# Kernel tuning notes

Measured on AMD Instinct MI355X. Metric: run time of the kernel, lower is better.

The kernel has to match this reference:

```python
import jax, jax.numpy as jnp
import numpy as np

N = 4096
BATCH = 256
N_IO = 16
EPS = 1.1920929e-07  # torch RMSNorm default eps = finfo(float32).eps


def setup_inputs() -> dict:
    key = jax.random.key(0)
    k_x, k_w = jax.random.split(key)
    x_input = jax.random.normal(k_x, (BATCH, N), dtype=jnp.float32)
    # orthogonal init for W
    a = jax.random.normal(k_w, (N, N), dtype=jnp.float32)
    q, r = jnp.linalg.qr(a)
    W = q * jnp.sign(jnp.diag(r))[None, :]
    B = jnp.zeros((N,), dtype=jnp.float32)
    input_scale = jnp.ones((N_IO,), dtype=jnp.float32)
    output_scale = jnp.ones((N_IO,), dtype=jnp.float32)
    norm_weight = jnp.ones((N,), dtype=jnp.float32)  # RMSNorm elementwise affine
    input_pos = jnp.arange(N_IO, dtype=jnp.int32)            # ids 0..15
    output_pos = jnp.arange(N_IO, dtype=jnp.int32) + (N - N_IO)  # ids 4080..4095
    return {
        "x_input": x_input, "W": W, "B": B,
        "input_scale": input_scale, "output_scale": output_scale,
        "norm_weight": norm_weight,
        "input_pos": input_pos, "output_pos": output_pos,
        "steps": 16,
    }


def reference(x_input, W, B, input_scale, output_scale, norm_weight,
              input_pos, output_pos, steps):
    # dropout is identity in eval mode (rate 0.0)
    def step(h, inj):
        signal = h @ W + B + inj                      # [batch, N]
        a = jnp.tanh(signal)
        ms = jnp.mean(a * a, axis=-1, keepdims=True)
        return a * jax.lax.rsqrt(ms + EPS) * norm_weight

    # pulse mode: scaled input injected only at t == 0
    inj0 = x_input.at[:, input_pos].multiply(input_scale)
    h0 = jnp.zeros_like(x_input)                      # fresh state
    h1 = step(h0, inj0)

    def body(h, _):
        hn = step(h, 0.0)
        return hn, hn

    h_final, rest = jax.lax.scan(body, h1, None, length=steps - 1)  # rest: [steps-1, batch, N]
    outs = jnp.concatenate([h1[:, None, :], jnp.swapaxes(rest, 0, 1)], axis=1)  # [batch, steps, N]
    outs = outs.at[:, :, output_pos].multiply(output_scale)
    return outs, h_final
```

## Files before the change

kernel.cpp:

```cpp
#include <hip/hip_runtime.h>
#include <hip/hip_bf16.h>

#define BATCH 256
#define NDIM  4096
#define STEPS 16
#define EPS_RMS 1.1920929e-07f

typedef _Float16 f16x8 __attribute__((ext_vector_type(8)));
typedef float  f32x4  __attribute__((ext_vector_type(4)));
typedef unsigned short u16x4 __attribute__((ext_vector_type(4)));
typedef unsigned int   u32x4 __attribute__((ext_vector_type(4)));

#define AS1 __attribute__((address_space(1)))
#define AS3 __attribute__((address_space(3)))
#define GLDS16(gp, lp) __builtin_amdgcn_global_load_lds( \
    (const AS1 void*)(gp), (AS3 void*)(lp), 16, 0, 0)
#define SBAR() do { asm volatile("" ::: "memory"); \
                    __builtin_amdgcn_s_barrier();  \
                    asm volatile("" ::: "memory"); } while (0)

__device__ __forceinline__ unsigned short f2h(float f) {
  _Float16 h = (_Float16)f;
  union { _Float16 h; unsigned short u; } v; v.h = h; return v.u;
}

__device__ __forceinline__ float block_reduce_sum_512(float v) {
  __shared__ float ws[8];
  __shared__ float tot;
  #pragma unroll
  for (int off = 32; off > 0; off >>= 1) v += __shfl_down(v, off, 64);
  int lane = threadIdx.x & 63, w = threadIdx.x >> 6;
  if (lane == 0) ws[w] = v;
  __syncthreads();
  if (threadIdx.x == 0) {
    float t = 0.f;
    #pragma unroll
    for (int i = 0; i < 8; ++i) t += ws[i];
    tot = t;
  }
  __syncthreads();
  return tot;
}

__global__ __launch_bounds__(256) void transpose_w(
    const float* __restrict__ W, unsigned short* __restrict__ Wt) {
  __shared__ float tile[64][65];
  int n0 = blockIdx.x * 64;
  int k0 = blockIdx.y * 64;
  int t = threadIdx.x;
  int r = t >> 4, c4 = (t & 15) * 4;
  #pragma unroll
  for (int p = 0; p < 4; ++p) {
    f32x4 v = *(const f32x4*)(W + (size_t)(k0 + r + 16 * p) * NDIM + n0 + c4);
    tile[r + 16 * p][c4 + 0] = v[0];
    tile[r + 16 * p][c4 + 1] = v[1];
    tile[r + 16 * p][c4 + 2] = v[2];
    tile[r + 16 * p][c4 + 3] = v[3];
  }
  __syncthreads();
  #pragma unroll
  for (int p = 0; p < 4; ++p) {
    int nr = r + 16 * p;
    u16x4 o;
    #pragma unroll
    for (int j = 0; j < 4; ++j) o[j] = f2h(tile[c4 + j][nr]);
    *(u16x4*)(Wt + (size_t)(n0 + nr) * NDIM + k0 + c4) = o;
  }
}

__global__ void init_colmul(const float* __restrict__ iscale,
                            const float* __restrict__ oscale,
                            const int* __restrict__ ipos, const int* __restrict__ opos,
                            float* __restrict__ icm, float* __restrict__ ocm) {
  int c = blockIdx.x * 256 + threadIdx.x;
  if (c >= NDIM) return;
  float iv = 1.f, ov = 1.f;
  #pragma unroll
  for (int i = 0; i < 16; ++i) {
    if (ipos[i] == c) iv *= iscale[i];
    if (opos[i] == c) ov *= oscale[i];
  }
  icm[c] = iv; ocm[c] = ov;
}

__global__ __launch_bounds__(512) void step0_kernel(
    const float* __restrict__ x, const float* __restrict__ bias,
    const float* __restrict__ icm, const float* __restrict__ nw,
    const float* __restrict__ ocm,
    unsigned short* __restrict__ hbuf, float* __restrict__ out) {
  int row = blockIdx.x;
  int tid = threadIdx.x;
  const float* xr = x + (size_t)row * NDIM;
  float a[8];
  float sq = 0.f;
  #pragma unroll
  for (int p = 0; p < 2; ++p) {
    int c = p * 2048 + tid * 4;
    f32x4 xv = *(const f32x4*)(xr + c);
    f32x4 bv = *(const f32x4*)(bias + c);
    f32x4 ic = *(const f32x4*)(icm + c);
    #pragma unroll
    for (int j = 0; j < 4; ++j) {
      float av = tanhf(bv[j] + xv[j] * ic[j]);
      a[p * 4 + j] = av;
      sq += av * av;
    }
  }
  float tot = block_reduce_sum_512(sq);
  float scale = rsqrtf(tot * (1.0f / NDIM) + EPS_RMS);
  unsigned short* hrow = hbuf + (size_t)row * NDIM;
  float* orow = out + (size_t)row * STEPS * NDIM;
  #pragma unroll
  for (int p = 0; p < 2; ++p) {
    int c = p * 2048 + tid * 4;
    f32x4 nv = *(const f32x4*)(nw + c);
    f32x4 oc = *(const f32x4*)(ocm + c);
    u16x4 hs; f32x4 os;
    #pragma unroll
    for (int j = 0; j < 4; ++j) {
      float h = a[p * 4 + j] * scale * nv[j];
      hs[j] = f2h(h);
      os[j] = h * oc[j];
    }
    *(u16x4*)(hrow + c) = hs;
    *(f32x4*)(orow + c) = os;
  }
}

__global__ __launch_bounds__(256, 2) void gemm_kernel(
    const unsigned short* __restrict__ A,
    const unsigned short* __restrict__ Bt,
    float* __restrict__ pbuf) {
  __shared__ __align__(16) unsigned short As[2][64 * 64];
  __shared__ __align__(16) unsigned short Bs[2][128 * 64];
  const int tid = threadIdx.x;
  const int n0 = blockIdx.x * 128;
  const int m0 = blockIdx.y * 64;
  const int ks = blockIdx.z;
  const int kbase = ks * 1024;
  const int wave = tid >> 6, lane = tid & 63;
  const int wm = (wave >> 1) * 32, wn = (wave & 1) * 64;
  const int l15 = lane & 15;
  const int g = lane >> 4;
  const int q = l15 & 7;
  const int rho = lane >> 3;
  const int koff = ((lane & 7) ^ rho) * 8;

  const unsigned short* aP[2];
  const unsigned short* bP[4];
  #pragma unroll
  for (int i = 0; i < 2; ++i)
    aP[i] = A + (size_t)(m0 + wave * 16 + i * 8 + rho) * NDIM + kbase + koff;
  #pragma unroll
  for (int i = 0; i < 4; ++i)
    bP[i] = Bt + (size_t)(n0 + wave * 32 + i * 8 + rho) * NDIM + kbase + koff;

  f32x4 acc[2][4];
  f32x4 zero = {0.f, 0.f, 0.f, 0.f};
  #pragma unroll
  for (int i = 0; i < 2; ++i)
    #pragma unroll
    for (int j = 0; j < 4; ++j) acc[i][j] = zero;

  #pragma unroll
  for (int i = 0; i < 2; ++i)
    GLDS16(aP[i], &As[0][(wave * 16 + i * 8) * 64]);
  #pragma unroll
  for (int i = 0; i < 4; ++i)
    GLDS16(bP[i], &Bs[0][(wave * 32 + i * 8) * 64]);

  for (int it = 0; it < 16; ++it) {
    const int p = it & 1;
    SBAR();
    if (it < 15) {
      const int kb = (it + 1) * 64;
      #pragma unroll
      for (int i = 0; i < 2; ++i)
        GLDS16(aP[i] + kb, &As[1 - p][(wave * 16 + i * 8) * 64]);
      #pragma unroll
      for (int i = 0; i < 4; ++i)
        GLDS16(bP[i] + kb, &Bs[1 - p][(wave * 32 + i * 8) * 64]);
      asm volatile("s_waitcnt vmcnt(6)" ::: "memory");
    } else {
      asm volatile("s_waitcnt vmcnt(0)" ::: "memory");
    }
    SBAR();
    #pragma unroll
    for (int kk = 0; kk < 2; ++kk) {
      f16x8 af[2], bfr[4];
      #pragma unroll
      for (int mf = 0; mf < 2; ++mf) {
        int row = wm + mf * 16 + l15;
        af[mf] = *(const f16x8*)&As[p][row * 64 + (((kk << 2) + g) ^ q) * 8];
      }
      #pragma unroll
      for (int nf = 0; nf < 4; ++nf) {
        int row = wn + nf * 16 + l15;
        bfr[nf] = *(const f16x8*)&Bs[p][row * 64 + (((kk << 2) + g) ^ q) * 8];
      }
      #pragma unroll
      for (int mf = 0; mf < 2; ++mf)
        #pragma unroll
        for (int nf = 0; nf < 4; ++nf)
          acc[mf][nf] = __builtin_amdgcn_mfma_f32_16x16x32_f16(af[mf], bfr[nf], acc[mf][nf], 0, 0, 0);
    }
  }

  float* pout = pbuf + (size_t)ks * BATCH * NDIM;
  const int crow = (lane >> 4) * 4;
  #pragma unroll
  for (int mf = 0; mf < 2; ++mf) {
    #pragma unroll
    for (int nf = 0; nf < 4; ++nf) {
      int col = n0 + wn + nf * 16 + l15;
      #pragma unroll
      for (int r = 0; r < 4; ++r) {
        int row = m0 + wm + mf * 16 + crow + r;
        pout[(size_t)row * NDIM + col] = acc[mf][nf][r];
      }
    }
  }
}

__global__ __launch_bounds__(512) void normalize_kernel(
    const float* __restrict__ pbuf, const float* __restrict__ bias,
    const float* __restrict__ nw, const float* __restrict__ ocm,
    unsigned short* __restrict__ hbuf, float* __restrict__ out,
    float* __restrict__ hfin, int t, int is_last) {
  const size_t SL = (size_t)BATCH * NDIM;
  int row = blockIdx.x;
  int tid = threadIdx.x;
  const float* p0 = pbuf + (size_t)row * NDIM;
  float a[8];
  float sq = 0.f;
  #pragma unroll
  for (int p = 0; p < 2; ++p) {
    int c = p * 2048 + tid * 4;
    f32x4 s = *(const f32x4*)(p0 + c);
    s += *(const f32x4*)(p0 + SL + c);
    s += *(const f32x4*)(p0 + 2 * SL + c);
    s += *(const f32x4*)(p0 + 3 * SL + c);
    f32x4 bv = *(const f32x4*)(bias + c);
    #pragma unroll
    for (int j = 0; j < 4; ++j) {
      float av = tanhf(s[j] + bv[j]);
      a[p * 4 + j] = av;
      sq += av * av;
    }
  }
  float tot = block_reduce_sum_512(sq);
  float scale = rsqrtf(tot * (1.0f / NDIM) + EPS_RMS);
  unsigned short* hrow = hbuf + (size_t)row * NDIM;
  float* orow = out + ((size_t)row * STEPS + t) * NDIM;
  #pragma unroll
  for (int p = 0; p < 2; ++p) {
    int c = p * 2048 + tid * 4;
    f32x4 nv = *(const f32x4*)(nw + c);
    f32x4 oc = *(const f32x4*)(ocm + c);
    u16x4 hs; f32x4 os; f32x4 hv;
    #pragma unroll
    for (int j = 0; j < 4; ++j) {
      float h = a[p * 4 + j] * scale * nv[j];
      hv[j] = h;
      hs[j] = f2h(h);
      os[j] = h * oc[j];
    }
    *(u16x4*)(hrow + c) = hs;
    *(f32x4*)(orow + c) = os;
    if (is_last) *(f32x4*)(hfin + (size_t)row * NDIM + c) = hv;
  }
}

extern "C" void kernel_launch(void* const* d_in, const int* in_sizes, int n_in,
                              void* d_out, int out_size, void* d_ws, size_t ws_size,
                              hipStream_t stream) {
  (void)in_sizes; (void)n_in; (void)out_size; (void)ws_size;
  const float* x      = (const float*)d_in[0];
  const float* W      = (const float*)d_in[1];
  const float* Bb     = (const float*)d_in[2];
  const float* iscale = (const float*)d_in[3];
  const float* oscale = (const float*)d_in[4];
  const float* nw     = (const float*)d_in[5];
  const int* ipos = (const int*)d_in[6];
  const int* opos = (const int*)d_in[7];

  char* ws = (char*)d_ws;
  unsigned short* Wt   = (unsigned short*)(ws);
  unsigned short* hbuf = (unsigned short*)(ws + 33554432);
  float* icm           = (float*)(ws + 35651584);
  float* ocm           = (float*)(ws + 35667968);
  float* pbuf          = (float*)(ws + 35684352);

  float* out  = (float*)d_out;
  float* hfin = out + (size_t)BATCH * STEPS * NDIM;

  hipLaunchKernelGGL(transpose_w, dim3(64, 64), dim3(256), 0, stream, W, Wt);
  hipLaunchKernelGGL(init_colmul, dim3(16), dim3(256), 0, stream,
                     iscale, oscale, ipos, opos, icm, ocm);
  hipLaunchKernelGGL(step0_kernel, dim3(256), dim3(512), 0, stream,
                     x, Bb, icm, nw, ocm, hbuf, out);
  for (int t = 1; t < STEPS; ++t) {
    hipLaunchKernelGGL(gemm_kernel, dim3(32, 4, 4), dim3(256), 0, stream,
                       hbuf, Wt, pbuf);
    hipLaunchKernelGGL(normalize_kernel, dim3(256), dim3(512), 0, stream,
                       pbuf, Bb, nw, ocm, hbuf, out, hfin, t, (t == STEPS - 1) ? 1 : 0);
  }
}
```

Measured before the change: 362.4 us.

## Fuse GEMM with tanh/RMS epilogue using deferred row normalization and atomic row sums

Replaces the split-K GEMM plus separate normalize kernel with one fused kernel per step. Each step stores the un-normalized tanh activations in fp16, accumulates squared sums per row with atomics, and applies the previous step's RMS scale inside the epilogue. This is valid because the row scale factors out of the matmul. Outputs for step t-1 are written lazily from the stored activations, and a final kernel handles the last step. This removes the fp32 partial-sum buffer traffic and half the launches. In exchange it drops split-K, so each step runs only 256 blocks of 128 threads over the full K=4096 loop, which may underutilize the GPU, and it relies on atomics.

```diff
diff --git a/kernel.cpp b/kernel.cpp
--- a/kernel.cpp
+++ b/kernel.cpp
@@ -9,6 +9,7 @@
 typedef _Float16 f16x8 __attribute__((ext_vector_type(8)));
 typedef float  f32x4  __attribute__((ext_vector_type(4)));
 typedef unsigned short u16x4 __attribute__((ext_vector_type(4)));
+typedef unsigned short u16x8 __attribute__((ext_vector_type(8)));
 typedef unsigned int   u32x4 __attribute__((ext_vector_type(4)));
 
 #define AS1 __attribute__((address_space(1)))
@@ -23,6 +24,9 @@
   _Float16 h = (_Float16)f;
   union { _Float16 h; unsigned short u; } v; v.h = h; return v.u;
 }
+__device__ __forceinline__ float h2f(unsigned short u) {
+  union { unsigned short u; _Float16 h; } v; v.u = u; return (float)v.h;
+}
 
 __device__ __forceinline__ float block_reduce_sum_512(float v) {
   __shared__ float ws[8];
@@ -71,9 +75,11 @@
 __global__ void init_colmul(const float* __restrict__ iscale,
                             const float* __restrict__ oscale,
                             const int* __restrict__ ipos, const int* __restrict__ opos,
-                            float* __restrict__ icm, float* __restrict__ ocm) {
+                            float* __restrict__ icm, float* __restrict__ ocm,
+                            float* __restrict__ rowsum) {
   int c = blockIdx.x * 256 + threadIdx.x;
   if (c >= NDIM) return;
+  rowsum[c] = 0.f;
   float iv = 1.f, ov = 1.f;
   #pragma unroll
   for (int i = 0; i < 16; ++i) {
@@ -86,8 +92,7 @@
 __global__ __launch_bounds__(512) void step0_kernel(
     const float* __restrict__ x, const float* __restrict__ bias,
     const float* __restrict__ icm, const float* __restrict__ nw,
-    const float* __restrict__ ocm,
-    unsigned short* __restrict__ hbuf, float* __restrict__ out) {
+    unsigned short* __restrict__ A0, float* __restrict__ rs0) {
   int row = blockIdx.x;
   int tid = threadIdx.x;
   const float* xr = x + (size_t)row * NDIM;
@@ -107,167 +112,185 @@
     }
   }
   float tot = block_reduce_sum_512(sq);
-  float scale = rsqrtf(tot * (1.0f / NDIM) + EPS_RMS);
-  unsigned short* hrow = hbuf + (size_t)row * NDIM;
-  float* orow = out + (size_t)row * STEPS * NDIM;
+  if (tid == 0) rs0[row] = tot;
+  unsigned short* arow = A0 + (size_t)row * NDIM;
   #pragma unroll
   for (int p = 0; p < 2; ++p) {
     int c = p * 2048 + tid * 4;
     f32x4 nv = *(const f32x4*)(nw + c);
-    f32x4 oc = *(const f32x4*)(ocm + c);
-    u16x4 hs; f32x4 os;
-    #pragma unroll
-    for (int j = 0; j < 4; ++j) {
-      float h = a[p * 4 + j] * scale * nv[j];
-      hs[j] = f2h(h);
-      os[j] = h * oc[j];
-    }
-    *(u16x4*)(hrow + c) = hs;
-    *(f32x4*)(orow + c) = os;
-  }
-}
-
-__global__ __launch_bounds__(256, 2) void gemm_kernel(
-    const unsigned short* __restrict__ A,
-    const unsigned short* __restrict__ Bt,
-    float* __restrict__ pbuf) {
+    u16x4 hs;
+    #pragma unroll
+    for (int j = 0; j < 4; ++j) hs[j] = f2h(a[p * 4 + j] * nv[j]);
+    *(u16x4*)(arow + c) = hs;
+  }
+}
+
+__global__ __launch_bounds__(128) void fused_step(
+    const unsigned short* __restrict__ Aprev,
+    unsigned short* __restrict__ Acur,
+    const unsigned short* __restrict__ Wt,
+    const float* __restrict__ bias, const float* __restrict__ nw,
+    const float* __restrict__ ocm,
+    const float* __restrict__ rs_prev, float* __restrict__ rs_cur,
+    float* __restrict__ out, int tm1) {
   __shared__ __align__(16) unsigned short As[2][64 * 64];
-  __shared__ __align__(16) unsigned short Bs[2][128 * 64];
+  __shared__ __align__(16) unsigned short Bs[2][64 * 64];
+  __shared__ float scale_s[64];
+
   const int tid = threadIdx.x;
-  const int n0 = blockIdx.x * 128;
+  const int n0 = blockIdx.x * 64;
   const int m0 = blockIdx.y * 64;
-  const int ks = blockIdx.z;
-  const int kbase = ks * 1024;
   const int wave = tid >> 6, lane = tid & 63;
-  const int wm = (wave >> 1) * 32, wn = (wave & 1) * 64;
+  const int wn = wave * 32;
   const int l15 = lane & 15;
   const int g = lane >> 4;
   const int q = l15 & 7;
-  const int rho = lane >> 3;
-  const int koff = ((lane & 7) ^ rho) * 8;
-
-  const unsigned short* aP[2];
+  const int srow = tid >> 3;
+  const int sch = tid & 7;
+  const int koff = (sch ^ (srow & 7)) * 8;
+
+  const unsigned short* aP[4];
   const unsigned short* bP[4];
   #pragma unroll
-  for (int i = 0; i < 2; ++i)
-    aP[i] = A + (size_t)(m0 + wave * 16 + i * 8 + rho) * NDIM + kbase + koff;
-  #pragma unroll
-  for (int i = 0; i < 4; ++i)
-    bP[i] = Bt + (size_t)(n0 + wave * 32 + i * 8 + rho) * NDIM + kbase + koff;
-
-  f32x4 acc[2][4];
+  for (int i = 0; i < 4; ++i) {
+    aP[i] = Aprev + (size_t)(m0 + i * 16 + srow) * NDIM + koff;
+    bP[i] = Wt + (size_t)(n0 + i * 16 + srow) * NDIM + koff;
+  }
+
+  f32x4 acc[4][2];
   f32x4 zero = {0.f, 0.f, 0.f, 0.f};
   #pragma unroll
-  for (int i = 0; i < 2; ++i)
-    #pragma unroll
-    for (int j = 0; j < 4; ++j) acc[i][j] = zero;
-
-  #pragma unroll
-  for (int i = 0; i < 2; ++i)
-    GLDS16(aP[i], &As[0][(wave * 16 + i * 8) * 64]);
-  #pragma unroll
-  for (int i = 0; i < 4; ++i)
-    GLDS16(bP[i], &Bs[0][(wave * 32 + i * 8) * 64]);
-
-  for (int it = 0; it < 16; ++it) {
+  for (int i = 0; i < 4; ++i) { acc[i][0] = zero; acc[i][1] = zero; }
+
+  #pragma unroll
+  for (int i = 0; i < 4; ++i) {
+    GLDS16(aP[i], &As[0][(i * 16 + srow) * 64 + sch * 8]);
+    GLDS16(bP[i], &Bs[0][(i * 16 + srow) * 64 + sch * 8]);
+  }
+
+  for (int it = 0; it < 64; ++it) {
     const int p = it & 1;
     SBAR();
-    if (it < 15) {
-      const int kb = (it + 1) * 64;
-      #pragma unroll
-      for (int i = 0; i < 2; ++i)
-        GLDS16(aP[i] + kb, &As[1 - p][(wave * 16 + i * 8) * 64]);
-      #pragma unroll
-      for (int i = 0; i < 4; ++i)
-        GLDS16(bP[i] + kb, &Bs[1 - p][(wave * 32 + i * 8) * 64]);
-      asm volatile("s_waitcnt vmcnt(6)" ::: "memory");
-    } else {
-      asm volatile("s_waitcnt vmcnt(0)" ::: "memory");
-    }
+    {
+      const int kb = (it < 63 ? (it + 1) : 63) * 64;
+      #pragma unroll
+      for (int i = 0; i < 4; ++i) {
+        GLDS16(aP[i] + kb, &As[1 - p][(i * 16 + srow) * 64 + sch * 8]);
+        GLDS16(bP[i] + kb, &Bs[1 - p][(i * 16 + srow) * 64 + sch * 8]);
+      }
+    }
+    asm volatile("s_waitcnt vmcnt(8)" ::: "memory");
     SBAR();
     #pragma unroll
     for (int kk = 0; kk < 2; ++kk) {
-      f16x8 af[2], bfr[4];
-      #pragma unroll
-      for (int mf = 0; mf < 2; ++mf) {
-        int row = wm + mf * 16 + l15;
-        af[mf] = *(const f16x8*)&As[p][row * 64 + (((kk << 2) + g) ^ q) * 8];
+      f16x8 af[4], bfr[2];
+      #pragma unroll
+      for (int mf = 0; mf < 4; ++mf)
+        af[mf] = *(const f16x8*)&As[p][(mf * 16 + l15) * 64 + (((kk << 2) + g) ^ q) * 8];
+      #pragma unroll
+      for (int nf = 0; nf < 2; ++nf)
+        bfr[nf] = *(const f16x8*)&Bs[p][(wn + nf * 16 + l15) * 64 + (((kk << 2) + g) ^ q) * 8];
+      #pragma unroll
+      for (int mf = 0; mf < 4; ++mf)
+        #pragma unroll
+        for (int nf = 0; nf < 2; ++nf)
+          acc[mf][nf] = __builtin_amdgcn_mfma_f32_16x16x32_f16(af[mf], bfr[nf], acc[mf][nf], 0, 0, 0);
+    }
+  }
+
+  __syncthreads();
+  if (tid < 64) scale_s[tid] = rsqrtf(rs_prev[m0 + tid] * (1.0f / NDIM) + EPS_RMS);
+  __syncthreads();
+
+  float bv[2], nwv[2];
+  #pragma unroll
+  for (int nf = 0; nf < 2; ++nf) {
+    bv[nf] = bias[n0 + wn + nf * 16 + l15];
+    nwv[nf] = nw[n0 + wn + nf * 16 + l15];
+  }
+  unsigned short* Ast = &As[0][0];
+
+  #pragma unroll
+  for (int mf = 0; mf < 4; ++mf) {
+    #pragma unroll
+    for (int r = 0; r < 4; ++r) {
+      int rl = mf * 16 + g * 4 + r;
+      float rp = scale_s[rl];
+      float s2 = 0.f;
+      #pragma unroll
+      for (int nf = 0; nf < 2; ++nf) {
+        float a = tanhf(acc[mf][nf][r] * rp + bv[nf]);
+        s2 += a * a;
+        Ast[rl * 64 + wn + nf * 16 + l15] = f2h(a * nwv[nf]);
       }
-      #pragma unroll
-      for (int nf = 0; nf < 4; ++nf) {
-        int row = wn + nf * 16 + l15;
-        bfr[nf] = *(const f16x8*)&Bs[p][row * 64 + (((kk << 2) + g) ^ q) * 8];
+      s2 += __shfl_xor(s2, 1, 64);
+      s2 += __shfl_xor(s2, 2, 64);
+      s2 += __shfl_xor(s2, 4, 64);
+      s2 += __shfl_xor(s2, 8, 64);
+      if (l15 == 0) atomicAdd(rs_cur + m0 + rl, s2);
+    }
+  }
+  __syncthreads();
+
+  {
+    int cl = (tid & 7) * 8;
+    #pragma unroll
+    for (int rd = 0; rd < 4; ++rd) {
+      int rl = rd * 16 + (tid >> 3);
+      *(u16x8*)(Acur + (size_t)(m0 + rl) * NDIM + n0 + cl) = *(u16x8*)&Ast[rl * 64 + cl];
+    }
+  }
+
+  {
+    int cl = (tid & 7) * 8;
+    f32x4 oc0 = *(const f32x4*)(ocm + n0 + cl);
+    f32x4 oc1 = *(const f32x4*)(ocm + n0 + cl + 4);
+    #pragma unroll
+    for (int rd = 0; rd < 4; ++rd) {
+      int rl = rd * 16 + (tid >> 3);
+      u16x8 av = *(const u16x8*)(Aprev + (size_t)(m0 + rl) * NDIM + n0 + cl);
+      float rp = scale_s[rl];
+      f32x4 o0, o1;
+      #pragma unroll
+      for (int j = 0; j < 4; ++j) {
+        o0[j] = h2f(av[j]) * rp * oc0[j];
+        o1[j] = h2f(av[j + 4]) * rp * oc1[j];
       }
-      #pragma unroll
-      for (int mf = 0; mf < 2; ++mf)
-        #pragma unroll
-        for (int nf = 0; nf < 4; ++nf)
-          acc[mf][nf] = __builtin_amdgcn_mfma_f32_16x16x32_f16(af[mf], bfr[nf], acc[mf][nf], 0, 0, 0);
-    }
-  }
-
-  float* pout = pbuf + (size_t)ks * BATCH * NDIM;
-  const int crow = (lane >> 4) * 4;
-  #pragma unroll
-  for (int mf = 0; mf < 2; ++mf) {
-    #pragma unroll
-    for (int nf = 0; nf < 4; ++nf) {
-      int col = n0 + wn + nf * 16 + l15;
-      #pragma unroll
-      for (int r = 0; r < 4; ++r) {
-        int row = m0 + wm + mf * 16 + crow + r;
-        pout[(size_t)row * NDIM + col] = acc[mf][nf][r];
-      }
-    }
-  }
-}
-
-__global__ __launch_bounds__(512) void normalize_kernel(
-    const float* __restrict__ pbuf, const float* __restrict__ bias,
-    const float* __restrict__ nw, const float* __restrict__ ocm,
-    unsigned short* __restrict__ hbuf, float* __restrict__ out,
-    float* __restrict__ hfin, int t, int is_last) {
-  const size_t SL = (size_t)BATCH * NDIM;
+      float* orow = out + ((size_t)(m0 + rl) * STEPS + tm1) * NDIM + n0 + cl;
+      *(f32x4*)orow = o0;
+      *(f32x4*)(orow + 4) = o1;
+    }
+  }
+}
+
+__global__ __launch_bounds__(256) void final_kernel(
+    const unsigned short* __restrict__ Alast, const float* __restrict__ rs15,
+    const float* __restrict__ ocm,
+    float* __restrict__ out, float* __restrict__ hfin) {
   int row = blockIdx.x;
   int tid = threadIdx.x;
-  const float* p0 = pbuf + (size_t)row * NDIM;
-  float a[8];
-  float sq = 0.f;
-  #pragma unroll
-  for (int p = 0; p < 2; ++p) {
-    int c = p * 2048 + tid * 4;
-    f32x4 s = *(const f32x4*)(p0 + c);
-    s += *(const f32x4*)(p0 + SL + c);
-    s += *(const f32x4*)(p0 + 2 * SL + c);
-    s += *(const f32x4*)(p0 + 3 * SL + c);
-    f32x4 bv = *(const f32x4*)(bias + c);
-    #pragma unroll
-    for (int j = 0; j < 4; ++j) {
-      float av = tanhf(s[j] + bv[j]);
-      a[p * 4 + j] = av;
-      sq += av * av;
-    }
-  }
-  float tot = block_reduce_sum_512(sq);
-  float scale = rsqrtf(tot * (1.0f / NDIM) + EPS_RMS);
-  unsigned short* hrow = hbuf + (size_t)row * NDIM;
-  float* orow = out + ((size_t)row * STEPS + t) * NDIM;
-  #pragma unroll
-  for (int p = 0; p < 2; ++p) {
-    int c = p * 2048 + tid * 4;
-    f32x4 nv = *(const f32x4*)(nw + c);
-    f32x4 oc = *(const f32x4*)(ocm + c);
-    u16x4 hs; f32x4 os; f32x4 hv;
-    #pragma unroll
-    for (int j = 0; j < 4; ++j) {
-      float h = a[p * 4 + j] * scale * nv[j];
-      hv[j] = h;
-      hs[j] = f2h(h);
-      os[j] = h * oc[j];
-    }
-    *(u16x4*)(hrow + c) = hs;
-    *(f32x4*)(orow + c) = os;
-    if (is_last) *(f32x4*)(hfin + (size_t)row * NDIM + c) = hv;
+  float rp = rsqrtf(rs15[row] * (1.0f / NDIM) + EPS_RMS);
+  const unsigned short* ar = Alast + (size_t)row * NDIM;
+  float* orow = out + ((size_t)row * STEPS + (STEPS - 1)) * NDIM;
+  float* frow = hfin + (size_t)row * NDIM;
+  #pragma unroll
+  for (int j = 0; j < 2; ++j) {
+    int c = tid * 16 + j * 8;
+    u16x8 av = *(const u16x8*)(ar + c);
+    f32x4 oc0 = *(const f32x4*)(ocm + c);
+    f32x4 oc1 = *(const f32x4*)(ocm + c + 4);
+    f32x4 h0, h1, o0, o1;
+    #pragma unroll
+    for (int k = 0; k < 4; ++k) {
+      h0[k] = h2f(av[k]) * rp;
+      h1[k] = h2f(av[k + 4]) * rp;
+      o0[k] = h0[k] * oc0[k];
+      o1[k] = h1[k] * oc1[k];
+    }
+    *(f32x4*)(orow + c) = o0;
+    *(f32x4*)(orow + c + 4) = o1;
+    *(f32x4*)(frow + c) = h0;
+    *(f32x4*)(frow + c + 4) = h1;
   }
 }
 
@@ -285,24 +308,28 @@
   const int* opos = (const int*)d_in[7];
 
   char* ws = (char*)d_ws;
-  unsigned short* Wt   = (unsigned short*)(ws);
-  unsigned short* hbuf = (unsigned short*)(ws + 33554432);
-  float* icm           = (float*)(ws + 35651584);
-  float* ocm           = (float*)(ws + 35667968);
-  float* pbuf          = (float*)(ws + 35684352);
+  unsigned short* Wt    = (unsigned short*)(ws);
+  unsigned short* abuf0 = (unsigned short*)(ws + 33554432);
+  unsigned short* abuf1 = (unsigned short*)(ws + 35651584);
+  float* icm            = (float*)(ws + 37748736);
+  float* ocm            = (float*)(ws + 37765120);
+  float* rowsum         = (float*)(ws + 37781504);
 
   float* out  = (float*)d_out;
   float* hfin = out + (size_t)BATCH * STEPS * NDIM;
 
   hipLaunchKernelGGL(transpose_w, dim3(64, 64), dim3(256), 0, stream, W, Wt);
   hipLaunchKernelGGL(init_colmul, dim3(16), dim3(256), 0, stream,
-                     iscale, oscale, ipos, opos, icm, ocm);
+                     iscale, oscale, ipos, opos, icm, ocm, rowsum);
   hipLaunchKernelGGL(step0_kernel, dim3(256), dim3(512), 0, stream,
-                     x, Bb, icm, nw, ocm, hbuf, out);
+                     x, Bb, icm, nw, abuf0, rowsum);
   for (int t = 1; t < STEPS; ++t) {
-    hipLaunchKernelGGL(gemm_kernel, dim3(32, 4, 4), dim3(256), 0, stream,
-                       hbuf, Wt, pbuf);
-    hipLaunchKernelGGL(normalize_kernel, dim3(256), dim3(512), 0, stream,
-                       pbuf, Bb, nw, ocm, hbuf, out, hfin, t, (t == STEPS - 1) ? 1 : 0);
-  }
-}
+    const unsigned short* Ap = ((t - 1) & 1) ? abuf1 : abuf0;
+    unsigned short* Ac = (t & 1) ? abuf1 : abuf0;
+    hipLaunchKernelGGL(fused_step, dim3(64, 4), dim3(128), 0, stream,
+                       Ap, Ac, Wt, Bb, nw, ocm,
+                       rowsum + (t - 1) * 256, rowsum + t * 256, out, t - 1);
+  }
+  hipLaunchKernelGGL(final_kernel, dim3(256), dim3(256), 0, stream,
+                     abuf1, rowsum + 15 * 256, ocm, out, hfin);
+}
```

Result: slower. 959.2 us (+164.7%).

## Enlarge GEMM tile to 128x128 and use deeper split-K when workspace allows

Applied to the files above, without the earlier changes.

The GEMM block tile grows from 64x128 to 128x128, so each wave computes 64x64 with 16 accumulators. This doubles operand reuse per LDS load and halves how often W is refetched across M blocks. To keep enough blocks in flight, split-K rises to 8 when the workspace is large enough, and the normalize kernel sums a variable number of partial slices. The cost is more partial-sum traffic in fp32, higher register pressure, and a runtime loop in the reduction.

```diff
diff --git a/kernel.cpp b/kernel.cpp
--- a/kernel.cpp
+++ b/kernel.cpp
@@ -130,66 +130,68 @@
 __global__ __launch_bounds__(256, 2) void gemm_kernel(
     const unsigned short* __restrict__ A,
     const unsigned short* __restrict__ Bt,
-    float* __restrict__ pbuf) {
-  __shared__ __align__(16) unsigned short As[2][64 * 64];
+    float* __restrict__ pbuf,
+    int kslen) {
+  __shared__ __align__(16) unsigned short As[2][128 * 64];
   __shared__ __align__(16) unsigned short Bs[2][128 * 64];
   const int tid = threadIdx.x;
   const int n0 = blockIdx.x * 128;
-  const int m0 = blockIdx.y * 64;
+  const int m0 = blockIdx.y * 128;
   const int ks = blockIdx.z;
-  const int kbase = ks * 1024;
+  const int kbase = ks * kslen;
+  const int nit = kslen >> 6;
   const int wave = tid >> 6, lane = tid & 63;
-  const int wm = (wave >> 1) * 32, wn = (wave & 1) * 64;
+  const int wm = (wave >> 1) * 64, wn = (wave & 1) * 64;
   const int l15 = lane & 15;
   const int g = lane >> 4;
   const int q = l15 & 7;
-  const int rho = lane >> 3;
-  const int koff = ((lane & 7) ^ rho) * 8;
-
-  const unsigned short* aP[2];
+  const int srow = tid >> 3;
+  const int sch = tid & 7;
+  const int koff = (sch ^ (srow & 7)) * 8;
+
+  const unsigned short* aP[4];
   const unsigned short* bP[4];
   #pragma unroll
-  for (int i = 0; i < 2; ++i)
-    aP[i] = A + (size_t)(m0 + wave * 16 + i * 8 + rho) * NDIM + kbase + koff;
+  for (int i = 0; i < 4; ++i) {
+    aP[i] = A + (size_t)(m0 + i * 32 + srow) * NDIM + kbase + koff;
+    bP[i] = Bt + (size_t)(n0 + i * 32 + srow) * NDIM + kbase + koff;
+  }
+
+  f32x4 acc[4][4];
+  f32x4 zero = {0.f, 0.f, 0.f, 0.f};
   #pragma unroll
   for (int i = 0; i < 4; ++i)
-    bP[i] = Bt + (size_t)(n0 + wave * 32 + i * 8 + rho) * NDIM + kbase + koff;
-
-  f32x4 acc[2][4];
-  f32x4 zero = {0.f, 0.f, 0.f, 0.f};
-  #pragma unroll
-  for (int i = 0; i < 2; ++i)
     #pragma unroll
     for (int j = 0; j < 4; ++j) acc[i][j] = zero;
 
   #pragma unroll
-  for (int i = 0; i < 2; ++i)
-    GLDS16(aP[i], &As[0][(wave * 16 + i * 8) * 64]);
-  #pragma unroll
   for (int i = 0; i < 4; ++i)
-    GLDS16(bP[i], &Bs[0][(wave * 32 + i * 8) * 64]);
-
-  for (int it = 0; it < 16; ++it) {
+    GLDS16(aP[i], &As[0][(i * 32 + srow) * 64 + sch * 8]);
+  #pragma unroll
+  for (int i = 0; i < 4; ++i)
+    GLDS16(bP[i], &Bs[0][(i * 32 + srow) * 64 + sch * 8]);
+
+  for (int it = 0; it < nit; ++it) {
     const int p = it & 1;
     SBAR();
-    if (it < 15) {
+    if (it < nit - 1) {
       const int kb = (it + 1) * 64;
       #pragma unroll
-      for (int i = 0; i < 2; ++i)
-        GLDS16(aP[i] + kb, &As[1 - p][(wave * 16 + i * 8) * 64]);
-      #pragma unroll
       for (int i = 0; i < 4; ++i)
-        GLDS16(bP[i] + kb, &Bs[1 - p][(wave * 32 + i * 8) * 64]);
-      asm volatile("s_waitcnt vmcnt(6)" ::: "memory");
+        GLDS16(aP[i] + kb, &As[1 - p][(i * 32 + srow) * 64 + sch * 8]);
+      #pragma unroll
+      for (int i = 0; i < 4; ++i)
+        GLDS16(bP[i] + kb, &Bs[1 - p][(i * 32 + srow) * 64 + sch * 8]);
+      asm volatile("s_waitcnt vmcnt(8)" ::: "memory");
     } else {
       asm volatile("s_waitcnt vmcnt(0)" ::: "memory");
     }
     SBAR();
     #pragma unroll
     for (int kk = 0; kk < 2; ++kk) {
-      f16x8 af[2], bfr[4];
-      #pragma unroll
-      for (int mf = 0; mf < 2; ++mf) {
+      f16x8 af[4], bfr[4];
+      #pragma unroll
+      for (int mf = 0; mf < 4; ++mf) {
         int row = wm + mf * 16 + l15;
         af[mf] = *(const f16x8*)&As[p][row * 64 + (((kk << 2) + g) ^ q) * 8];
       }
@@ -199,7 +201,7 @@
         bfr[nf] = *(const f16x8*)&Bs[p][row * 64 + (((kk << 2) + g) ^ q) * 8];
       }
       #pragma unroll
-      for (int mf = 0; mf < 2; ++mf)
+      for (int mf = 0; mf < 4; ++mf)
         #pragma unroll
         for (int nf = 0; nf < 4; ++nf)
           acc[mf][nf] = __builtin_amdgcn_mfma_f32_16x16x32_f16(af[mf], bfr[nf], acc[mf][nf], 0, 0, 0);
@@ -207,9 +209,9 @@
   }
 
   float* pout = pbuf + (size_t)ks * BATCH * NDIM;
-  const int crow = (lane >> 4) * 4;
-  #pragma unroll
-  for (int mf = 0; mf < 2; ++mf) {
+  const int crow = g * 4;
+  #pragma unroll
+  for (int mf = 0; mf < 4; ++mf) {
     #pragma unroll
     for (int nf = 0; nf < 4; ++nf) {
       int col = n0 + wn + nf * 16 + l15;
@@ -226,7 +228,7 @@
     const float* __restrict__ pbuf, const float* __restrict__ bias,
     const float* __restrict__ nw, const float* __restrict__ ocm,
     unsigned short* __restrict__ hbuf, float* __restrict__ out,
-    float* __restrict__ hfin, int t, int is_last) {
+    float* __restrict__ hfin, int t, int is_last, int ksplit) {
   const size_t SL = (size_t)BATCH * NDIM;
   int row = blockIdx.x;
   int tid = threadIdx.x;
@@ -237,9 +239,8 @@
   for (int p = 0; p < 2; ++p) {
     int c = p * 2048 + tid * 4;
     f32x4 s = *(const f32x4*)(p0 + c);
-    s += *(const f32x4*)(p0 + SL + c);
-    s += *(const f32x4*)(p0 + 2 * SL + c);
-    s += *(const f32x4*)(p0 + 3 * SL + c);
+    for (int k = 1; k < ksplit; ++k)
+      s += *(const f32x4*)(p0 + (size_t)k * SL + c);
     f32x4 bv = *(const f32x4*)(bias + c);
     #pragma unroll
     for (int j = 0; j < 4; ++j) {
@@ -274,7 +275,7 @@
 extern "C" void kernel_launch(void* const* d_in, const int* in_sizes, int n_in,
                               void* d_out, int out_size, void* d_ws, size_t ws_size,
                               hipStream_t stream) {
-  (void)in_sizes; (void)n_in; (void)out_size; (void)ws_size;
+  (void)in_sizes; (void)n_in; (void)out_size;
   const float* x      = (const float*)d_in[0];
   const float* W      = (const float*)d_in[1];
   const float* Bb     = (const float*)d_in[2];
@@ -291,6 +292,10 @@
   float* ocm           = (float*)(ws + 35667968);
   float* pbuf          = (float*)(ws + 35684352);
 
+  size_t need8 = 35684352 + (size_t)8 * BATCH * NDIM * sizeof(float);
+  int ksplit = (ws_size >= need8) ? 8 : 4;
+  int kslen = NDIM / ksplit;
+
   float* out  = (float*)d_out;
   float* hfin = out + (size_t)BATCH * STEPS * NDIM;
 
@@ -300,9 +305,10 @@
   hipLaunchKernelGGL(step0_kernel, dim3(256), dim3(512), 0, stream,
                      x, Bb, icm, nw, ocm, hbuf, out);
   for (int t = 1; t < STEPS; ++t) {
-    hipLaunchKernelGGL(gemm_kernel, dim3(32, 4, 4), dim3(256), 0, stream,
-                       hbuf, Wt, pbuf);
+    hipLaunchKernelGGL(gemm_kernel, dim3(32, 2, ksplit), dim3(256), 0, stream,
+                       hbuf, Wt, pbuf, kslen);
     hipLaunchKernelGGL(normalize_kernel, dim3(256), dim3(512), 0, stream,
-                       pbuf, Bb, nw, ocm, hbuf, out, hfin, t, (t == STEPS - 1) ? 1 : 0);
-  }
-}
+                       pbuf, Bb, nw, ocm, hbuf, out, hfin, t,
+                       (t == STEPS - 1) ? 1 : 0, ksplit);
+  }
+}
```

Measured after the change: 403.6 us. 11.4% more time.

## Triple-buffer GEMM LDS tiles and fold column-scale init into transpose

Applied to the files above, without the earlier changes.

The GEMM k-loop moves from double to triple buffering in LDS. Loads are issued two tiles ahead, and one of the two barriers per iteration is dropped, so more global-load latency is hidden and there is less synchronisation. Separately, the init_colmul kernel is merged into transpose_w, which removes one launch. Triple buffering raises LDS use per block from 48KB to 72KB, which may limit how many blocks fit per CU.

```diff
diff --git a/kernel.cpp b/kernel.cpp
--- a/kernel.cpp
+++ b/kernel.cpp
@@ -43,11 +43,24 @@
 }
 
 __global__ __launch_bounds__(256) void transpose_w(
-    const float* __restrict__ W, unsigned short* __restrict__ Wt) {
+    const float* __restrict__ W, unsigned short* __restrict__ Wt,
+    const float* __restrict__ iscale, const float* __restrict__ oscale,
+    const int* __restrict__ ipos, const int* __restrict__ opos,
+    float* __restrict__ icm, float* __restrict__ ocm) {
   __shared__ float tile[64][65];
   int n0 = blockIdx.x * 64;
   int k0 = blockIdx.y * 64;
   int t = threadIdx.x;
+  if (blockIdx.y == 0 && t < 64) {
+    int c = n0 + t;
+    float iv = 1.f, ov = 1.f;
+    #pragma unroll
+    for (int i = 0; i < 16; ++i) {
+      if (ipos[i] == c) iv *= iscale[i];
+      if (opos[i] == c) ov *= oscale[i];
+    }
+    icm[c] = iv; ocm[c] = ov;
+  }
   int r = t >> 4, c4 = (t & 15) * 4;
   #pragma unroll
   for (int p = 0; p < 4; ++p) {
@@ -66,21 +79,6 @@
     for (int j = 0; j < 4; ++j) o[j] = f2h(tile[c4 + j][nr]);
     *(u16x4*)(Wt + (size_t)(n0 + nr) * NDIM + k0 + c4) = o;
   }
-}
-
-__global__ void init_colmul(const float* __restrict__ iscale,
-                            const float* __restrict__ oscale,
-                            const int* __restrict__ ipos, const int* __restrict__ opos,
-                            float* __restrict__ icm, float* __restrict__ ocm) {
-  int c = blockIdx.x * 256 + threadIdx.x;
-  if (c >= NDIM) return;
-  float iv = 1.f, ov = 1.f;
-  #pragma unroll
-  for (int i = 0; i < 16; ++i) {
-    if (ipos[i] == c) iv *= iscale[i];
-    if (opos[i] == c) ov *= oscale[i];
-  }
-  icm[c] = iv; ocm[c] = ov;
 }
 
 __global__ __launch_bounds__(512) void step0_kernel(
@@ -131,8 +129,8 @@
     const unsigned short* __restrict__ A,
     const unsigned short* __restrict__ Bt,
     float* __restrict__ pbuf) {
-  __shared__ __align__(16) unsigned short As[2][64 * 64];
-  __shared__ __align__(16) unsigned short Bs[2][128 * 64];
+  __shared__ __align__(16) unsigned short As[3][64 * 64];
+  __shared__ __align__(16) unsigned short Bs[3][128 * 64];
   const int tid = threadIdx.x;
   const int n0 = blockIdx.x * 128;
   const int m0 = blockIdx.y * 64;
@@ -163,40 +161,44 @@
     for (int j = 0; j < 4; ++j) acc[i][j] = zero;
 
   #pragma unroll
-  for (int i = 0; i < 2; ++i)
-    GLDS16(aP[i], &As[0][(wave * 16 + i * 8) * 64]);
-  #pragma unroll
-  for (int i = 0; i < 4; ++i)
-    GLDS16(bP[i], &Bs[0][(wave * 32 + i * 8) * 64]);
-
+  for (int b = 0; b < 2; ++b) {
+    #pragma unroll
+    for (int i = 0; i < 2; ++i)
+      GLDS16(aP[i] + b * 64, &As[b][(wave * 16 + i * 8) * 64]);
+    #pragma unroll
+    for (int i = 0; i < 4; ++i)
+      GLDS16(bP[i] + b * 64, &Bs[b][(wave * 32 + i * 8) * 64]);
+  }
+
+  int pr = 0, pw = 2;
   for (int it = 0; it < 16; ++it) {
-    const int p = it & 1;
     SBAR();
-    if (it < 15) {
-      const int kb = (it + 1) * 64;
+    if (it < 14) {
+      const int kb = (it + 2) * 64;
       #pragma unroll
       for (int i = 0; i < 2; ++i)
-        GLDS16(aP[i] + kb, &As[1 - p][(wave * 16 + i * 8) * 64]);
+        GLDS16(aP[i] + kb, &As[pw][(wave * 16 + i * 8) * 64]);
       #pragma unroll
       for (int i = 0; i < 4; ++i)
-        GLDS16(bP[i] + kb, &Bs[1 - p][(wave * 32 + i * 8) * 64]);
+        GLDS16(bP[i] + kb, &Bs[pw][(wave * 32 + i * 8) * 64]);
+      asm volatile("s_waitcnt vmcnt(12)" ::: "memory");
+    } else if (it == 14) {
       asm volatile("s_waitcnt vmcnt(6)" ::: "memory");
     } else {
       asm volatile("s_waitcnt vmcnt(0)" ::: "memory");
     }
-    SBAR();
     #pragma unroll
     for (int kk = 0; kk < 2; ++kk) {
       f16x8 af[2], bfr[4];
       #pragma unroll
       for (int mf = 0; mf < 2; ++mf) {
         int row = wm + mf * 16 + l15;
-        af[mf] = *(const f16x8*)&As[p][row * 64 + (((kk << 2) + g) ^ q) * 8];
+        af[mf] = *(const f16x8*)&As[pr][row * 64 + (((kk << 2) + g) ^ q) * 8];
       }
       #pragma unroll
       for (int nf = 0; nf < 4; ++nf) {
         int row = wn + nf * 16 + l15;
-        bfr[nf] = *(const f16x8*)&Bs[p][row * 64 + (((kk << 2) + g) ^ q) * 8];
+        bfr[nf] = *(const f16x8*)&Bs[pr][row * 64 + (((kk << 2) + g) ^ q) * 8];
       }
       #pragma unroll
       for (int mf = 0; mf < 2; ++mf)
@@ -204,6 +206,8 @@
         for (int nf = 0; nf < 4; ++nf)
           acc[mf][nf] = __builtin_amdgcn_mfma_f32_16x16x32_f16(af[mf], bfr[nf], acc[mf][nf], 0, 0, 0);
     }
+    pr = (pr == 2) ? 0 : pr + 1;
+    pw = (pw == 2) ? 0 : pw + 1;
   }
 
   float* pout = pbuf + (size_t)ks * BATCH * NDIM;
@@ -294,9 +298,8 @@
   float* out  = (float*)d_out;
   float* hfin = out + (size_t)BATCH * STEPS * NDIM;
 
-  hipLaunchKernelGGL(transpose_w, dim3(64, 64), dim3(256), 0, stream, W, Wt);
-  hipLaunchKernelGGL(init_colmul, dim3(16), dim3(256), 0, stream,
-                     iscale, oscale, ipos, opos, icm, ocm);
+  hipLaunchKernelGGL(transpose_w, dim3(64, 64), dim3(256), 0, stream,
+                     W, Wt, iscale, oscale, ipos, opos, icm, ocm);
   hipLaunchKernelGGL(step0_kernel, dim3(256), dim3(512), 0, stream,
                      x, Bb, icm, nw, ocm, hbuf, out);
   for (int t = 1; t < STEPS; ++t) {
```

Result: slower. 373.3 us (+3.0%).
